# Kernel optimization log

Hardware: AMD Instinct MI355X
Metric: run time of the kernel (lower is better)

The kernel has to match this reference:

```python
import jax, jax.numpy as jnp
import numpy as np

N, E, B, D, F_IN, E_IN, H = 8192, 32768, 256, 64, 11, 5, 128


def setup_inputs() -> dict:
    key = jax.random.key(0)
    ks = jax.random.split(key, 32)
    rn = lambda k, shape, s: jax.random.normal(k, shape, jnp.float32) * s
    inp = {
        'x': jax.random.normal(ks[0], (N, F_IN), jnp.float32),
        'edge_attr': jax.random.uniform(ks[1], (E, E_IN), jnp.float32),
        'lin0_w': rn(ks[2], (D, F_IN), 0.3), 'lin0_b': jnp.zeros((D,), jnp.float32),
        'nn1_w': rn(ks[3], (H, E_IN), 0.4), 'nn1_b': jnp.zeros((H,), jnp.float32),
        'nn2_w': rn(ks[4], (D * D, H), 0.05), 'nn2_b': jnp.zeros((D * D,), jnp.float32),
        'root_w': rn(ks[5], (D, D), 0.125), 'conv_b': jnp.zeros((D,), jnp.float32),
        'gru_w_ih': rn(ks[6], (3 * D, D), 0.125), 'gru_w_hh': rn(ks[7], (3 * D, D), 0.125),
        'gru_b_ih': jnp.zeros((3 * D,), jnp.float32), 'gru_b_hh': jnp.zeros((3 * D,), jnp.float32),
        's2s_w_ih': rn(ks[8], (4 * D, 2 * D), 0.1), 's2s_w_hh': rn(ks[9], (4 * D, D), 0.125),
        's2s_b_ih': jnp.zeros((4 * D,), jnp.float32), 's2s_b_hh': jnp.zeros((4 * D,), jnp.float32),
        'lin1_w': rn(ks[10], (D, 2 * D), 0.1), 'lin1_b': jnp.zeros((D,), jnp.float32),
        'lin2_w': rn(ks[11], (1, D), 0.125), 'lin2_b': jnp.zeros((1,), jnp.float32),
        'edge_index': jax.random.randint(ks[12], (2, E), 0, N),
        'batch': jnp.sort(jax.random.randint(ks[13], (N,), 0, B)),
    }
    return inp


def _forward(x, edge_attr, lin0_w, lin0_b, nn1_w, nn1_b, nn2_w, nn2_b, root_w, conv_b,
             gru_w_ih, gru_w_hh, gru_b_ih, gru_b_hh, s2s_w_ih, s2s_w_hh, s2s_b_ih, s2s_b_hh,
             lin1_w, lin1_b, lin2_w, lin2_b, edge_index, batch):
    src, dst = edge_index[0], edge_index[1]
    # edge-conditioned weights: MLP(edge_attr) -> [E, D, D]; edge_attr is fixed,
    # so compute once (identical math to calling conv.nn each iteration)
    W_e = (jax.nn.relu(edge_attr @ nn1_w.T + nn1_b) @ nn2_w.T + nn2_b).reshape(E, D, D)
    deg = jax.ops.segment_sum(jnp.ones((E,), jnp.float32), dst, num_segments=N)
    inv_deg = jnp.where(deg > 0, 1.0 / jnp.maximum(deg, 1.0), 0.0)[:, None]  # [N,1]

    out = jax.nn.relu(x @ lin0_w.T + lin0_b)  # [N, D]
    h = out
    for _ in range(3):
        # NNConv: gather src features, per-edge matmul, scatter-mean to dst, + root + bias
        msg = jnp.einsum('ed,edf->ef', out[src], W_e)  # [E, D]
        agg = jax.ops.segment_sum(msg, dst, num_segments=N) * inv_deg
        m = jax.nn.relu(agg + out @ root_w.T + conv_b)
        # single-step GRU (torch GRU equations)
        gx = m @ gru_w_ih.T + gru_b_ih
        gh = h @ gru_w_hh.T + gru_b_hh
        xr, xz, xn = jnp.split(gx, 3, axis=-1)
        hr, hz, hn = jnp.split(gh, 3, axis=-1)
        r = jax.nn.sigmoid(xr + hr)
        z = jax.nn.sigmoid(xz + hz)
        n = jnp.tanh(xn + r * hn)
        h = (1.0 - z) * n + z * h
        out = h

    # Set2Set pooling, 3 processing steps
    qh = jnp.zeros((B, D), jnp.float32)
    qc = jnp.zeros((B, D), jnp.float32)
    q_star = jnp.zeros((B, 2 * D), jnp.float32)
    for _ in range(3):
        gates = q_star @ s2s_w_ih.T + s2s_b_ih + qh @ s2s_w_hh.T + s2s_b_hh
        gi, gf, gg, go = jnp.split(gates, 4, axis=-1)
        qc = jax.nn.sigmoid(gf) * qc + jax.nn.sigmoid(gi) * jnp.tanh(gg)
        qh = jax.nn.sigmoid(go) * jnp.tanh(qc)
        q = qh  # [B, D]
        e = jnp.sum(out * q[batch], axis=-1)  # [N]
        emax = jax.ops.segment_max(e, batch, num_segments=B)
        emax = jnp.where(jnp.isfinite(emax), emax, 0.0)
        a = jnp.exp(e - emax[batch])
        a_sum = jax.ops.segment_sum(a, batch, num_segments=B)
        a = a / jnp.maximum(a_sum, 1e-12)[batch]
        r_vec = jax.ops.segment_sum(a[:, None] * out, batch, num_segments=B)  # [B, D]
        q_star = jnp.concatenate([q, r_vec], axis=-1)

    y = jax.nn.relu(q_star @ lin1_w.T + lin1_b) @ lin2_w.T + lin2_b
    return y.reshape(-1)  # [B]


def reference(x, edge_attr, lin0_w, lin0_b, nn1_w, nn1_b, nn2_w, nn2_b, root_w, conv_b,
              gru_w_ih, gru_w_hh, gru_b_ih, gru_b_hh, s2s_w_ih, s2s_w_hh, s2s_b_ih, s2s_b_hh,
              lin1_w, lin1_b, lin2_w, lin2_b, edge_index, batch):
    return _forward(x, edge_attr, lin0_w, lin0_b, nn1_w, nn1_b, nn2_w, nn2_b, root_w, conv_b,
                    gru_w_ih, gru_w_hh, gru_b_ih, gru_b_hh, s2s_w_ih, s2s_w_hh, s2s_b_ih, s2s_b_hh,
                    lin1_w, lin1_b, lin2_w, lin2_b, edge_index, batch)
```

## Files before the change

kernel.cpp:

```cpp
#include <hip/hip_runtime.h>
#include <hip/hip_bf16.h>
#include <stdint.h>

#define NN 8192
#define EE 32768
#define BB 256
#define DD 64
#define FIN 11
#define EIN 5
#define HH 128

typedef __attribute__((ext_vector_type(4))) float f32x4;
typedef __attribute__((ext_vector_type(8))) short bf16x8;

__device__ __forceinline__ float sigmoidf_(float x) { return 1.0f / (1.0f + expf(-x)); }

__device__ __forceinline__ void gload16(const void* g, void* l) {
    __builtin_amdgcn_global_load_lds(
        (const __attribute__((address_space(1))) unsigned int*)g,
        (__attribute__((address_space(3))) unsigned int*)l, 16, 0, 0);
}

__global__ __launch_bounds__(256) void k_setup(const float* __restrict__ x,
                                               const float* __restrict__ edge_attr,
                                               const float* __restrict__ lin0_w,
                                               const float* __restrict__ lin0_b,
                                               const float* __restrict__ nn1_w,
                                               const float* __restrict__ nn1_b,
                                               const float* __restrict__ nn2_w,
                                               const float* __restrict__ nn2b,
                                               const float* __restrict__ root_w,
                                               const float* __restrict__ whh,
                                               const float* __restrict__ bhh,
                                               const float* __restrict__ s2s_wih,
                                               const float* __restrict__ s2s_whh,
                                               const int* __restrict__ ei,
                                               const int* __restrict__ batch,
                                               __hip_bfloat16* __restrict__ h1,
                                               float* __restrict__ outN,
                                               __hip_bfloat16* __restrict__ nn2T,
                                               float* __restrict__ wihT,
                                               float* __restrict__ whhT,
                                               float* __restrict__ Bcat,
                                               float* __restrict__ bcat,
                                               int* __restrict__ deg,
                                               int* __restrict__ cnt) {
    const int bid = blockIdx.x, t = threadIdx.x;
    if (bid < 16384) {
        int idx = bid * 256 + t;
        int e = idx >> 7, k = idx & 127;
        float a = nn1_b[k];
#pragma unroll
        for (int j = 0; j < EIN; j++) a += edge_attr[e * EIN + j] * nn1_w[k * EIN + j];
        h1[idx] = __float2bfloat16(fmaxf(a, 0.0f));
    } else if (bid < 18432) {
        int idx = (bid - 16384) * 256 + t;
        int n = idx >> 6, d = idx & 63;
        float a = lin0_b[d];
#pragma unroll
        for (int k = 0; k < FIN; k++) a += x[n * FIN + k] * lin0_w[d * FIN + k];
        outN[idx] = fmaxf(a, 0.0f);
    } else if (bid < 18688) {
        int u = (bid - 18432) * 256 + t;
        int d = u >> 10, rem = u & 1023, slot = rem >> 6, f = rem & 63;
        const float* src = nn2_w + ((size_t)(d * 64 + f) * 128 + slot * 8);
        float4 v0 = *(const float4*)(src);
        float4 v1 = *(const float4*)(src + 4);
        union { bf16x8 v; ushort us[8]; } ov;
        __hip_bfloat16 b;
        b = __float2bfloat16(v0.x); ov.us[0] = *(ushort*)&b;
        b = __float2bfloat16(v0.y); ov.us[1] = *(ushort*)&b;
        b = __float2bfloat16(v0.z); ov.us[2] = *(ushort*)&b;
        b = __float2bfloat16(v0.w); ov.us[3] = *(ushort*)&b;
        b = __float2bfloat16(v1.x); ov.us[4] = *(ushort*)&b;
        b = __float2bfloat16(v1.y); ov.us[5] = *(ushort*)&b;
        b = __float2bfloat16(v1.z); ov.us[6] = *(ushort*)&b;
        b = __float2bfloat16(v1.w); ov.us[7] = *(ushort*)&b;
        *(bf16x8*)((ushort*)nn2T + (size_t)u * 8) = ov.v;
    } else if (bid < 18880) {
        int i = (bid - 18688) * 256 + t;
        if (i < 256 * 128) {
            int j = i >> 7, k = i & 127;
            wihT[k * 256 + j] = s2s_wih[i];
        } else {
            int i2 = i - 256 * 128;
            if (i2 < 256 * 64) {
                int j = i2 >> 6, k = i2 & 63;
                whhT[k * 256 + j] = s2s_whh[i2];
            }
        }
    } else if (bid < 18960) {
        int i = (bid - 18880) * 256 + t;
        int r = i >> 6, c = i & 63;
        float v;
        if (r < 64) v = root_w[i];
        else if (r < 256) v = whh[(size_t)(r - 64) * 64 + c];
        else v = nn2b[c * 64 + (r - 256)];
        Bcat[i] = v;
        if (c == 0) bcat[r] = (r >= 64 && r < 256) ? bhh[r - 64] : 0.0f;
    } else {
        int i = (bid - 18960) * 256 + t;
        if (i < EE) atomicAdd(&deg[ei[EE + i]], 1);
        if (i < NN) atomicAdd(&cnt[batch[i]], 1);
    }
}

__global__ __launch_bounds__(256) void k_invscan(const int* __restrict__ deg,
                                                 float* __restrict__ invd,
                                                 const int* __restrict__ cnt,
                                                 int* __restrict__ offs) {
    const int bid = blockIdx.x, t = threadIdx.x;
    if (bid < 32) {
        int n = bid * 256 + t;
        int d = deg[n];
        invd[n] = d > 0 ? 1.0f / (float)d : 0.0f;
    } else {
        __shared__ int s[256];
        s[t] = cnt[t];
        __syncthreads();
        for (int off = 1; off < 256; off <<= 1) {
            int v = (t >= off) ? s[t - off] : 0;
            __syncthreads();
            s[t] += v;
            __syncthreads();
        }
        offs[t + 1] = s[t];
        if (t == 0) offs[0] = 0;
    }
}

__global__ __launch_bounds__(512, 6) void k_wemsg(const __hip_bfloat16* __restrict__ h1,
                                                  const __hip_bfloat16* __restrict__ nn2T,
                                                  const float* __restrict__ outN,
                                                  const float* __restrict__ rgh,
                                                  const int* __restrict__ ei,
                                                  const float* __restrict__ invd,
                                                  float* __restrict__ agg) {
    __shared__ ushort sB[2][64 * 128];
    __shared__ float soT[32][64];
    __shared__ int sDst[64];
    __shared__ int sSrc[64];
    __shared__ float sIv[64];

    const int t = threadIdx.x;
    const int w = t >> 6, l = t & 63;
    const int q = l >> 4, l15 = l & 15;
    const int eh = w >> 2, fs = (w & 3) * 16;
    const int e0 = (blockIdx.x >> 1) * 64;
    const int dh = blockIdx.x & 1;
    const int cbase = dh * 32;

    {
        int r = t >> 3, seg = t & 7;
        int s_ = ei[e0 + r];
        float4 v = *(const float4*)(outN + (size_t)s_ * 64 + dh * 32 + seg * 4);
        soT[seg * 4 + 0][r] = v.x;
        soT[seg * 4 + 1][r] = v.y;
        soT[seg * 4 + 2][r] = v.z;
        soT[seg * 4 + 3][r] = v.w;
        if (seg == 0) {
            int d_ = ei[EE + e0 + r];
            sDst[r] = d_;
            sIv[r] = invd[d_];
            sSrc[r] = s_;
        }
    }
    bf16x8 af[2][4];
#pragma unroll
    for (int mi = 0; mi < 2; mi++)
#pragma unroll
        for (int kk = 0; kk < 4; kk++)
            af[mi][kk] = *(const bf16x8*)(h1 + (size_t)(e0 + eh * 32 + mi * 16 + l15) * 128 + (kk * 4 + q) * 8);

    const __hip_bfloat16* p0 = nn2T + (size_t)cbase * 8192 + (size_t)t * 8;
    const __hip_bfloat16* p1 = nn2T + (size_t)cbase * 8192 + (size_t)(512 + t) * 8;
    ushort* d0a = &sB[0][(w * 64) * 8];
    ushort* d0b = &sB[0][(512 + w * 64) * 8];
    ushort* d1a = &sB[1][(w * 64) * 8];
    ushort* d1b = &sB[1][(512 + w * 64) * 8];

    gload16(p0, d0a);
    gload16(p1, d0b);
    __syncthreads();

    float msg[2][4];
#pragma unroll
    for (int mi = 0; mi < 2; mi++)
#pragma unroll
        for (int j = 0; j < 4; j++) msg[mi][j] = 0.0f;

    const int rb = fs + l15;
    const int lo0 = ((0 * 4 + q) * 64 + rb) * 8;
    const int lo1 = ((1 * 4 + q) * 64 + rb) * 8;
    const int lo2 = ((2 * 4 + q) * 64 + rb) * 8;
    const int lo3 = ((3 * 4 + q) * 64 + rb) * 8;

    for (int dl = 0; dl < 32; ++dl) {
        const int cur = dl & 1;
        if (dl < 31) {
            size_t off = (size_t)(dl + 1) * 8192;
            gload16(p0 + off, cur ? d0a : d1a);
            gload16(p1 + off, cur ? d0b : d1b);
        }
        const ushort* sbc = &sB[cur][0];
        f32x4 a0 = (f32x4)0.0f, a1 = (f32x4)0.0f;
        {
            bf16x8 b0_ = *(const bf16x8*)&sbc[lo0];
            a0 = __builtin_amdgcn_mfma_f32_16x16x32_bf16(af[0][0], b0_, a0, 0, 0, 0);
            a1 = __builtin_amdgcn_mfma_f32_16x16x32_bf16(af[1][0], b0_, a1, 0, 0, 0);
            bf16x8 b1_ = *(const bf16x8*)&sbc[lo1];
            a0 = __builtin_amdgcn_mfma_f32_16x16x32_bf16(af[0][1], b1_, a0, 0, 0, 0);
            a1 = __builtin_amdgcn_mfma_f32_16x16x32_bf16(af[1][1], b1_, a1, 0, 0, 0);
            bf16x8 b2_ = *(const bf16x8*)&sbc[lo2];
            a0 = __builtin_amdgcn_mfma_f32_16x16x32_bf16(af[0][2], b2_, a0, 0, 0, 0);
            a1 = __builtin_amdgcn_mfma_f32_16x16x32_bf16(af[1][2], b2_, a1, 0, 0, 0);
            bf16x8 b3_ = *(const bf16x8*)&sbc[lo3];
            a0 = __builtin_amdgcn_mfma_f32_16x16x32_bf16(af[0][3], b3_, a0, 0, 0, 0);
            a1 = __builtin_amdgcn_mfma_f32_16x16x32_bf16(af[1][3], b3_, a1, 0, 0, 0);
        }
        {
            f32x4 s0 = *(const f32x4*)&soT[dl][eh * 32 + q * 4];
            f32x4 s1 = *(const f32x4*)&soT[dl][eh * 32 + 16 + q * 4];
#pragma unroll
            for (int j = 0; j < 4; j++) {
                msg[0][j] += a0[j] * s0[j];
                msg[1][j] += a1[j] * s1[j];
            }
        }
        __syncthreads();
    }

    const int fcol = fs + l15;
#pragma unroll
    for (int mi = 0; mi < 2; mi++) {
#pragma unroll
        for (int j = 0; j < 4; j++) {
            int er = eh * 32 + mi * 16 + q * 4 + j;
            float v = msg[mi][j];
            if (dh == 0) v += rgh[(size_t)sSrc[er] * 320 + 256 + fcol];
            atomicAdd(&agg[(size_t)sDst[er] * 64 + fcol], v * sIv[er]);
        }
    }
}

__global__ __launch_bounds__(256) void k_rgh(const float* __restrict__ A,
                                             const float* __restrict__ Bm,
                                             const float* __restrict__ bias,
                                             float* __restrict__ C,
                                             float* __restrict__ aggz) {
    const int tid = threadIdx.x;
    const int bx = blockIdx.x, by = blockIdx.y;
    {
        int bid = by * 5 + bx;
        if (bid < 512) {
            float4 z; z.x = z.y = z.z = z.w = 0.0f;
            *(float4*)(aggz + (size_t)bid * 1024 + tid * 4) = z;
        }
    }
    __shared__ float sA[64 * 68];
    __shared__ float sB[64 * 68];
    const float* Ab = A + (size_t)by * 64 * 64;
    const float* Bb = Bm + (size_t)bx * 64 * 64;
    for (int fi = tid; fi < 64 * 16; fi += 256) {
        int r = fi >> 4, c = (fi & 15) * 4;
        *(float4*)&sA[r * 68 + c] = *(const float4*)(Ab + (size_t)r * 64 + c);
        *(float4*)&sB[r * 68 + c] = *(const float4*)(Bb + (size_t)r * 64 + c);
    }
    __syncthreads();
    const int tx = tid & 15, ty = tid >> 4;
    float acc[4][4];
#pragma unroll
    for (int i = 0; i < 4; i++)
#pragma unroll
        for (int j = 0; j < 4; j++) acc[i][j] = 0.0f;
    for (int k = 0; k < 64; k += 4) {
        float4 av[4], bv[4];
#pragma unroll
        for (int i = 0; i < 4; i++) av[i] = *(const float4*)&sA[(ty + 16 * i) * 68 + k];
#pragma unroll
        for (int j = 0; j < 4; j++) bv[j] = *(const float4*)&sB[(tx + 16 * j) * 68 + k];
#pragma unroll
        for (int i = 0; i < 4; i++)
#pragma unroll
            for (int j = 0; j < 4; j++) {
                acc[i][j] += av[i].x * bv[j].x;
                acc[i][j] += av[i].y * bv[j].y;
                acc[i][j] += av[i].z * bv[j].z;
                acc[i][j] += av[i].w * bv[j].w;
            }
    }
#pragma unroll
    for (int i = 0; i < 4; i++) {
        size_t row = (size_t)by * 64 + ty + 16 * i;
#pragma unroll
        for (int j = 0; j < 4; j++) {
            int col = bx * 64 + tx + 16 * j;
            C[row * 320 + col] = acc[i][j] + bias[col];
        }
    }
}

__global__ __launch_bounds__(256) void k_gxgru(const float* __restrict__ agg,
                                               const float* __restrict__ rgh,
                                               const float* __restrict__ cb,
                                               const float* __restrict__ wih,
                                               const float* __restrict__ bih,
                                               float* __restrict__ outN) {
    __shared__ float sA[64 * 68];
    __shared__ float sB[192 * 68];
    const int t = threadIdx.x;
    const int by = blockIdx.x;
    for (int fi = t; fi < 64 * 16; fi += 256) {
        int r = fi >> 4, c = (fi & 15) * 4;
        float4 av = *(const float4*)(agg + (size_t)(by * 64 + r) * 64 + c);
        float4 rv = *(const float4*)(rgh + (size_t)(by * 64 + r) * 320 + c);
        float4 cv = *(const float4*)(cb + c);
        float4 m;
        m.x = fmaxf(av.x + rv.x + cv.x, 0.0f);
        m.y = fmaxf(av.y + rv.y + cv.y, 0.0f);
        m.z = fmaxf(av.z + rv.z + cv.z, 0.0f);
        m.w = fmaxf(av.w + rv.w + cv.w, 0.0f);
        *(float4*)&sA[r * 68 + c] = m;
    }
    for (int fi = t; fi < 192 * 16; fi += 256) {
        int r = fi >> 4, c = (fi & 15) * 4;
        *(float4*)&sB[r * 68 + c] = *(const float4*)(wih + (size_t)r * 64 + c);
    }
    __syncthreads();
    const int tx = t & 15, ty = t >> 4;
    float acc[3][4][4];
#pragma unroll
    for (int cx = 0; cx < 3; cx++)
#pragma unroll
        for (int i = 0; i < 4; i++)
#pragma unroll
            for (int j = 0; j < 4; j++) acc[cx][i][j] = 0.0f;
    for (int k = 0; k < 64; k += 4) {
        float4 av[4];
#pragma unroll
        for (int i = 0; i < 4; i++) av[i] = *(const float4*)&sA[(ty + 16 * i) * 68 + k];
#pragma unroll
        for (int cx = 0; cx < 3; cx++) {
            float4 bv[4];
#pragma unroll
            for (int j = 0; j < 4; j++) bv[j] = *(const float4*)&sB[(cx * 64 + tx + 16 * j) * 68 + k];
#pragma unroll
            for (int i = 0; i < 4; i++)
#pragma unroll
                for (int j = 0; j < 4; j++) {
                    acc[cx][i][j] += av[i].x * bv[j].x;
                    acc[cx][i][j] += av[i].y * bv[j].y;
                    acc[cx][i][j] += av[i].z * bv[j].z;
                    acc[cx][i][j] += av[i].w * bv[j].w;
                }
        }
    }
#pragma unroll
    for (int i = 0; i < 4; i++) {
        int n = by * 64 + ty + 16 * i;
        const float* ghr = rgh + (size_t)n * 320 + 64;
#pragma unroll
        for (int j = 0; j < 4; j++) {
            int d = tx + 16 * j;
            float r = sigmoidf_(acc[0][i][j] + bih[d] + ghr[d]);
            float z = sigmoidf_(acc[1][i][j] + bih[64 + d] + ghr[64 + d]);
            float nn_ = tanhf(acc[2][i][j] + bih[128 + d] + r * ghr[128 + d]);
            float hp = outN[(size_t)n * 64 + d];
            outN[(size_t)n * 64 + d] = (1.0f - z) * nn_ + z * hp;
        }
    }
}

__global__ __launch_bounds__(256) void k_s2sall(const float* __restrict__ outN,
                                                const int* __restrict__ offs,
                                                const float* __restrict__ wihT,
                                                const float* __restrict__ whhT,
                                                const float* __restrict__ bih,
                                                const float* __restrict__ bhh,
                                                const float* __restrict__ lin1_w,
                                                const float* __restrict__ lin1_b,
                                                const float* __restrict__ lin2_w,
                                                const float* __restrict__ lin2_b,
                                                float* __restrict__ earr,
                                                float* __restrict__ y) {
    const int b = blockIdx.x, t = threadIdx.x;
    const int w = t >> 6, l = t & 63;
    __shared__ float qs[128], qhL[64], qcL[64], gates[256];
    __shared__ float red[8];
    __shared__ float rpart[4][64];
    __shared__ float hbuf[64];
    const int s0 = offs[b], s1 = offs[b + 1];
    if (t < 128) qs[t] = 0.0f;
    if (t < 64) { qhL[t] = 0.0f; qcL[t] = 0.0f; }
    __syncthreads();

    for (int st = 0; st < 3; st++) {
        float g = bih[t] + bhh[t];
        for (int k = 0; k < 128; k++) g += qs[k] * wihT[k * 256 + t];
        for (int k = 0; k < 64; k++) g += qhL[k] * whhT[k * 256 + t];
        gates[t] = g;
        __syncthreads();
        if (t < 64) {
            float gi = gates[t], gf = gates[64 + t], gg = gates[128 + t], go = gates[192 + t];
            float c = sigmoidf_(gf) * qcL[t] + sigmoidf_(gi) * tanhf(gg);
            qcL[t] = c;
            qhL[t] = sigmoidf_(go) * tanhf(c);
        }
        __syncthreads();
        float mx = -INFINITY;
        for (int i = s0 + w; i < s1; i += 4) {
            float p = outN[(size_t)i * 64 + l] * qhL[l];
#pragma unroll
            for (int o = 32; o > 0; o >>= 1) p += __shfl_xor(p, o, 64);
            if (l == 0) earr[i] = p;
            mx = fmaxf(mx, p);
        }
        if (l == 0) red[w] = mx;
        __syncthreads();
        mx = fmaxf(fmaxf(red[0], red[1]), fmaxf(red[2], red[3]));
        if (!isfinite(mx)) mx = 0.0f;
        float sm = 0.0f, racc = 0.0f;
        for (int i = s0 + w; i < s1; i += 4) {
            float a = expf(earr[i] - mx);
            sm += a;
            racc += a * outN[(size_t)i * 64 + l];
        }
        rpart[w][l] = racc;
        if (l == 0) red[4 + w] = sm;
        __syncthreads();
        float smT = fmaxf(red[4] + red[5] + red[6] + red[7], 1e-12f);
        if (t < 64) {
            float r = (rpart[0][t] + rpart[1][t] + rpart[2][t] + rpart[3][t]) / smT;
            qs[t] = qhL[t];
            qs[64 + t] = r;
        }
        __syncthreads();
    }
    if (t < 64) {
        float h = lin1_b[t];
        for (int k = 0; k < 128; k++) h += qs[k] * lin1_w[t * 128 + k];
        hbuf[t] = fmaxf(h, 0.0f) * lin2_w[t];
    }
    __syncthreads();
    if (w == 0) {
        float p = hbuf[l];
#pragma unroll
        for (int o = 32; o > 0; o >>= 1) p += __shfl_xor(p, o, 64);
        if (l == 0) y[b] = p + lin2_b[0];
    }
}

extern "C" void kernel_launch(void* const* d_in, const int* in_sizes, int n_in,
                              void* d_out, int out_size, void* d_ws, size_t ws_size,
                              hipStream_t stream) {
    const float* x = (const float*)d_in[0];
    const float* edge_attr = (const float*)d_in[1];
    const float* lin0_w = (const float*)d_in[2];
    const float* lin0_b = (const float*)d_in[3];
    const float* nn1_w = (const float*)d_in[4];
    const float* nn1_b = (const float*)d_in[5];
    const float* nn2_w = (const float*)d_in[6];
    const float* nn2_b = (const float*)d_in[7];
    const float* root_w = (const float*)d_in[8];
    const float* conv_b = (const float*)d_in[9];
    const float* gru_w_ih = (const float*)d_in[10];
    const float* gru_w_hh = (const float*)d_in[11];
    const float* gru_b_ih = (const float*)d_in[12];
    const float* gru_b_hh = (const float*)d_in[13];
    const float* s2s_w_ih = (const float*)d_in[14];
    const float* s2s_w_hh = (const float*)d_in[15];
    const float* s2s_b_ih = (const float*)d_in[16];
    const float* s2s_b_hh = (const float*)d_in[17];
    const float* lin1_w = (const float*)d_in[18];
    const float* lin1_b = (const float*)d_in[19];
    const float* lin2_w = (const float*)d_in[20];
    const float* lin2_b = (const float*)d_in[21];
    const int* ei = (const int*)d_in[22];
    const int* batch = (const int*)d_in[23];
    float* outp = (float*)d_out;

    char* w = (char*)d_ws;
    auto carve = [&](size_t bytes) { char* p = w; w += (bytes + 255) & ~(size_t)255; return p; };
    __hip_bfloat16* nn2T = (__hip_bfloat16*)carve((size_t)4096 * 128 * 2);
    float* outN = (float*)carve((size_t)NN * 64 * 4);
    __hip_bfloat16* h1 = (__hip_bfloat16*)carve((size_t)EE * 128 * 2);
    int* deg = (int*)carve(NN * 4);
    float* invd = (float*)carve(NN * 4);
    float* agg = (float*)carve((size_t)NN * 64 * 4);
    float* rgh = (float*)carve((size_t)NN * 320 * 4);
    float* Bcat = (float*)carve((size_t)320 * 64 * 4);
    float* bcat = (float*)carve(320 * 4);
    float* wihT = (float*)carve((size_t)128 * 256 * 4);
    float* whhT = (float*)carve((size_t)64 * 256 * 4);
    float* earr = (float*)carve(NN * 4);
    int* cnt = (int*)carve(256 * 4);
    int* offs = (int*)carve(257 * 4);

    hipMemsetAsync(deg, 0, NN * 4, stream);
    hipMemsetAsync(cnt, 0, 256 * 4, stream);

    k_setup<<<19088, 256, 0, stream>>>(x, edge_attr, lin0_w, lin0_b, nn1_w, nn1_b,
                                       nn2_w, nn2_b, root_w, gru_w_hh, gru_b_hh,
                                       s2s_w_ih, s2s_w_hh, ei, batch,
                                       h1, outN, nn2T, wihT, whhT, Bcat, bcat, deg, cnt);
    k_invscan<<<33, 256, 0, stream>>>(deg, invd, cnt, offs);

    for (int it = 0; it < 3; it++) {
        k_rgh<<<dim3(5, NN / 64), 256, 0, stream>>>(outN, Bcat, bcat, rgh, agg);
        k_wemsg<<<EE / 32, 512, 0, stream>>>(h1, nn2T, outN, rgh, ei, invd, agg);
        k_gxgru<<<NN / 64, 256, 0, stream>>>(agg, rgh, conv_b, gru_w_ih, gru_b_ih, outN);
    }

    k_s2sall<<<BB, 256, 0, stream>>>(outN, offs, wihT, whhT, s2s_b_ih, s2s_b_hh,
                                     lin1_w, lin1_b, lin2_w, lin2_b, earr, outp);
}
```

Before: 321.8 us.

## Halve wemsg block to 256 threads with 4 edge tiles per wave; vectorize setup

The edge-message kernel now runs 4 waves per block instead of 8, and each wave computes all 64 edges (four 16-row MFMA tiles) for its 16 output columns. Each B fragment read from LDS is therefore reused across four MFMAs instead of two, which cuts LDS traffic per FLOP. The cost is more accumulator and A-fragment registers per wave and fewer waves per block to hide latency. Separately, the setup kernel computes 4 outputs per thread with vector stores for h1 and outN, which reduces its block count.

Result: slower. 336.7 us (+4.6%).

```diff
diff --git a/kernel.cpp b/kernel.cpp
--- a/kernel.cpp
+++ b/kernel.cpp
@@ -46,22 +46,41 @@
                                                int* __restrict__ deg,
                                                int* __restrict__ cnt) {
     const int bid = blockIdx.x, t = threadIdx.x;
-    if (bid < 16384) {
-        int idx = bid * 256 + t;
-        int e = idx >> 7, k = idx & 127;
-        float a = nn1_b[k];
-#pragma unroll
-        for (int j = 0; j < EIN; j++) a += edge_attr[e * EIN + j] * nn1_w[k * EIN + j];
-        h1[idx] = __float2bfloat16(fmaxf(a, 0.0f));
-    } else if (bid < 18432) {
-        int idx = (bid - 16384) * 256 + t;
-        int n = idx >> 6, d = idx & 63;
-        float a = lin0_b[d];
-#pragma unroll
-        for (int k = 0; k < FIN; k++) a += x[n * FIN + k] * lin0_w[d * FIN + k];
-        outN[idx] = fmaxf(a, 0.0f);
-    } else if (bid < 18688) {
-        int u = (bid - 18432) * 256 + t;
+    if (bid < 4096) {
+        int u = bid * 256 + t;
+        int e = u >> 5, k0 = (u & 31) * 4;
+        float ea0 = edge_attr[e * EIN + 0], ea1 = edge_attr[e * EIN + 1],
+              ea2 = edge_attr[e * EIN + 2], ea3 = edge_attr[e * EIN + 3],
+              ea4 = edge_attr[e * EIN + 4];
+        ushort4 o;
+#pragma unroll
+        for (int kk = 0; kk < 4; kk++) {
+            int k = k0 + kk;
+            const float* wr = nn1_w + k * EIN;
+            float a = nn1_b[k] + ea0 * wr[0] + ea1 * wr[1] + ea2 * wr[2] + ea3 * wr[3] + ea4 * wr[4];
+            __hip_bfloat16 b = __float2bfloat16(fmaxf(a, 0.0f));
+            ((ushort*)&o)[kk] = *(ushort*)&b;
+        }
+        *(ushort4*)((ushort*)h1 + (size_t)e * 128 + k0) = o;
+    } else if (bid < 4608) {
+        int u = (bid - 4096) * 256 + t;
+        int n = u >> 4, d0 = (u & 15) * 4;
+        float xv[FIN];
+#pragma unroll
+        for (int k = 0; k < FIN; k++) xv[k] = x[n * FIN + k];
+        float4 o;
+#pragma unroll
+        for (int dd = 0; dd < 4; dd++) {
+            int d = d0 + dd;
+            const float* wr = lin0_w + d * FIN;
+            float a = lin0_b[d];
+#pragma unroll
+            for (int k = 0; k < FIN; k++) a += xv[k] * wr[k];
+            ((float*)&o)[dd] = fmaxf(a, 0.0f);
+        }
+        *(float4*)(outN + (size_t)n * 64 + d0) = o;
+    } else if (bid < 4864) {
+        int u = (bid - 4608) * 256 + t;
         int d = u >> 10, rem = u & 1023, slot = rem >> 6, f = rem & 63;
         const float* src = nn2_w + ((size_t)(d * 64 + f) * 128 + slot * 8);
         float4 v0 = *(const float4*)(src);
@@ -77,8 +96,8 @@
         b = __float2bfloat16(v1.z); ov.us[6] = *(ushort*)&b;
         b = __float2bfloat16(v1.w); ov.us[7] = *(ushort*)&b;
         *(bf16x8*)((ushort*)nn2T + (size_t)u * 8) = ov.v;
-    } else if (bid < 18880) {
-        int i = (bid - 18688) * 256 + t;
+    } else if (bid < 5056) {
+        int i = (bid - 4864) * 256 + t;
         if (i < 256 * 128) {
             int j = i >> 7, k = i & 127;
             wihT[k * 256 + j] = s2s_wih[i];
@@ -89,8 +108,8 @@
                 whhT[k * 256 + j] = s2s_whh[i2];
             }
         }
-    } else if (bid < 18960) {
-        int i = (bid - 18880) * 256 + t;
+    } else if (bid < 5136) {
+        int i = (bid - 5056) * 256 + t;
         int r = i >> 6, c = i & 63;
         float v;
         if (r < 64) v = root_w[i];
@@ -99,7 +118,7 @@
         Bcat[i] = v;
         if (c == 0) bcat[r] = (r >= 64 && r < 256) ? bhh[r - 64] : 0.0f;
     } else {
-        int i = (bid - 18960) * 256 + t;
+        int i = (bid - 5136) * 256 + t;
         if (i < EE) atomicAdd(&deg[ei[EE + i]], 1);
         if (i < NN) atomicAdd(&cnt[batch[i]], 1);
     }
@@ -129,7 +148,7 @@
     }
 }
 
-__global__ __launch_bounds__(512, 6) void k_wemsg(const __hip_bfloat16* __restrict__ h1,
+__global__ __launch_bounds__(256, 3) void k_wemsg(const __hip_bfloat16* __restrict__ h1,
                                                   const __hip_bfloat16* __restrict__ nn2T,
                                                   const float* __restrict__ outN,
                                                   const float* __restrict__ rgh,
@@ -145,19 +164,25 @@
     const int t = threadIdx.x;
     const int w = t >> 6, l = t & 63;
     const int q = l >> 4, l15 = l & 15;
-    const int eh = w >> 2, fs = (w & 3) * 16;
     const int e0 = (blockIdx.x >> 1) * 64;
     const int dh = blockIdx.x & 1;
     const int cbase = dh * 32;
 
     {
-        int r = t >> 3, seg = t & 7;
+        int r = t >> 2, seg = t & 3;
         int s_ = ei[e0 + r];
-        float4 v = *(const float4*)(outN + (size_t)s_ * 64 + dh * 32 + seg * 4);
-        soT[seg * 4 + 0][r] = v.x;
-        soT[seg * 4 + 1][r] = v.y;
-        soT[seg * 4 + 2][r] = v.z;
-        soT[seg * 4 + 3][r] = v.w;
+        const float* orow = outN + (size_t)s_ * 64 + dh * 32 + seg * 8;
+        float4 v0 = *(const float4*)(orow);
+        float4 v1 = *(const float4*)(orow + 4);
+        int c0 = seg * 8;
+        soT[c0 + 0][r] = v0.x;
+        soT[c0 + 1][r] = v0.y;
+        soT[c0 + 2][r] = v0.z;
+        soT[c0 + 3][r] = v0.w;
+        soT[c0 + 4][r] = v1.x;
+        soT[c0 + 5][r] = v1.y;
+        soT[c0 + 6][r] = v1.z;
+        soT[c0 + 7][r] = v1.w;
         if (seg == 0) {
             int d_ = ei[EE + e0 + r];
             sDst[r] = d_;
@@ -165,31 +190,26 @@
             sSrc[r] = s_;
         }
     }
-    bf16x8 af[2][4];
-#pragma unroll
-    for (int mi = 0; mi < 2; mi++)
+    bf16x8 af[4][4];
+#pragma unroll
+    for (int mi = 0; mi < 4; mi++)
 #pragma unroll
         for (int kk = 0; kk < 4; kk++)
-            af[mi][kk] = *(const bf16x8*)(h1 + (size_t)(e0 + eh * 32 + mi * 16 + l15) * 128 + (kk * 4 + q) * 8);
-
-    const __hip_bfloat16* p0 = nn2T + (size_t)cbase * 8192 + (size_t)t * 8;
-    const __hip_bfloat16* p1 = nn2T + (size_t)cbase * 8192 + (size_t)(512 + t) * 8;
-    ushort* d0a = &sB[0][(w * 64) * 8];
-    ushort* d0b = &sB[0][(512 + w * 64) * 8];
-    ushort* d1a = &sB[1][(w * 64) * 8];
-    ushort* d1b = &sB[1][(512 + w * 64) * 8];
-
-    gload16(p0, d0a);
-    gload16(p1, d0b);
+            af[mi][kk] = *(const bf16x8*)(h1 + (size_t)(e0 + mi * 16 + l15) * 128 + (kk * 4 + q) * 8);
+
+    const __hip_bfloat16* pst = nn2T + (size_t)cbase * 8192 + (size_t)t * 8;
+#pragma unroll
+    for (int i = 0; i < 4; i++)
+        gload16(pst + i * 2048, &sB[0][(i * 256 + w * 64) * 8]);
     __syncthreads();
 
-    float msg[2][4];
-#pragma unroll
-    for (int mi = 0; mi < 2; mi++)
+    float msg[4][4];
+#pragma unroll
+    for (int mi = 0; mi < 4; mi++)
 #pragma unroll
         for (int j = 0; j < 4; j++) msg[mi][j] = 0.0f;
 
-    const int rb = fs + l15;
+    const int rb = w * 16 + l15;
     const int lo0 = ((0 * 4 + q) * 64 + rb) * 8;
     const int lo1 = ((1 * 4 + q) * 64 + rb) * 8;
     const int lo2 = ((2 * 4 + q) * 64 + rb) * 8;
@@ -199,43 +219,57 @@
         const int cur = dl & 1;
         if (dl < 31) {
             size_t off = (size_t)(dl + 1) * 8192;
-            gload16(p0 + off, cur ? d0a : d1a);
-            gload16(p1 + off, cur ? d0b : d1b);
+            ushort* db = cur ? &sB[0][0] : &sB[1][0];
+#pragma unroll
+            for (int i = 0; i < 4; i++)
+                gload16(pst + off + i * 2048, db + (i * 256 + w * 64) * 8);
         }
         const ushort* sbc = &sB[cur][0];
-        f32x4 a0 = (f32x4)0.0f, a1 = (f32x4)0.0f;
+        f32x4 a0 = (f32x4)0.0f, a1 = (f32x4)0.0f, a2 = (f32x4)0.0f, a3 = (f32x4)0.0f;
         {
             bf16x8 b0_ = *(const bf16x8*)&sbc[lo0];
             a0 = __builtin_amdgcn_mfma_f32_16x16x32_bf16(af[0][0], b0_, a0, 0, 0, 0);
             a1 = __builtin_amdgcn_mfma_f32_16x16x32_bf16(af[1][0], b0_, a1, 0, 0, 0);
+            a2 = __builtin_amdgcn_mfma_f32_16x16x32_bf16(af[2][0], b0_, a2, 0, 0, 0);
+            a3 = __builtin_amdgcn_mfma_f32_16x16x32_bf16(af[3][0], b0_, a3, 0, 0, 0);
             bf16x8 b1_ = *(const bf16x8*)&sbc[lo1];
             a0 = __builtin_amdgcn_mfma_f32_16x16x32_bf16(af[0][1], b1_, a0, 0, 0, 0);
             a1 = __builtin_amdgcn_mfma_f32_16x16x32_bf16(af[1][1], b1_, a1, 0, 0, 0);
+            a2 = __builtin_amdgcn_mfma_f32_16x16x32_bf16(af[2][1], b1_, a2, 0, 0, 0);
+            a3 = __builtin_amdgcn_mfma_f32_16x16x32_bf16(af[3][1], b1_, a3, 0, 0, 0);
             bf16x8 b2_ = *(const bf16x8*)&sbc[lo2];
             a0 = __builtin_amdgcn_mfma_f32_16x16x32_bf16(af[0][2], b2_, a0, 0, 0, 0);
             a1 = __builtin_amdgcn_mfma_f32_16x16x32_bf16(af[1][2], b2_, a1, 0, 0, 0);
+            a2 = __builtin_amdgcn_mfma_f32_16x16x32_bf16(af[2][2], b2_, a2, 0, 0, 0);
+            a3 = __builtin_amdgcn_mfma_f32_16x16x32_bf16(af[3][2], b2_, a3, 0, 0, 0);
             bf16x8 b3_ = *(const bf16x8*)&sbc[lo3];
             a0 = __builtin_amdgcn_mfma_f32_16x16x32_bf16(af[0][3], b3_, a0, 0, 0, 0);
             a1 = __builtin_amdgcn_mfma_f32_16x16x32_bf16(af[1][3], b3_, a1, 0, 0, 0);
+            a2 = __builtin_amdgcn_mfma_f32_16x16x32_bf16(af[2][3], b3_, a2, 0, 0, 0);
+            a3 = __builtin_amdgcn_mfma_f32_16x16x32_bf16(af[3][3], b3_, a3, 0, 0, 0);
         }
         {
-            f32x4 s0 = *(const f32x4*)&soT[dl][eh * 32 + q * 4];
-            f32x4 s1 = *(const f32x4*)&soT[dl][eh * 32 + 16 + q * 4];
+            f32x4 s0 = *(const f32x4*)&soT[dl][0 * 16 + q * 4];
+            f32x4 s1 = *(const f32x4*)&soT[dl][1 * 16 + q * 4];
+            f32x4 s2 = *(const f32x4*)&soT[dl][2 * 16 + q * 4];
+            f32x4 s3 = *(const f32x4*)&soT[dl][3 * 16 + q * 4];
 #pragma unroll
             for (int j = 0; j < 4; j++) {
                 msg[0][j] += a0[j] * s0[j];
                 msg[1][j] += a1[j] * s1[j];
+                msg[2][j] += a2[j] * s2[j];
+                msg[3][j] += a3[j] * s3[j];
             }
         }
         __syncthreads();
     }
 
-    const int fcol = fs + l15;
-#pragma unroll
-    for (int mi = 0; mi < 2; mi++) {
+    const int fcol = w * 16 + l15;
+#pragma unroll
+    for (int mi = 0; mi < 4; mi++) {
 #pragma unroll
         for (int j = 0; j < 4; j++) {
-            int er = eh * 32 + mi * 16 + q * 4 + j;
+            int er = mi * 16 + q * 4 + j;
             float v = msg[mi][j];
             if (dh == 0) v += rgh[(size_t)sSrc[er] * 320 + 256 + fcol];
             atomicAdd(&agg[(size_t)sDst[er] * 64 + fcol], v * sIv[er]);
@@ -499,15 +533,15 @@
     hipMemsetAsync(deg, 0, NN * 4, stream);
     hipMemsetAsync(cnt, 0, 256 * 4, stream);
 
-    k_setup<<<19088, 256, 0, stream>>>(x, edge_attr, lin0_w, lin0_b, nn1_w, nn1_b,
-                                       nn2_w, nn2_b, root_w, gru_w_hh, gru_b_hh,
-                                       s2s_w_ih, s2s_w_hh, ei, batch,
-                                       h1, outN, nn2T, wihT, whhT, Bcat, bcat, deg, cnt);
+    k_setup<<<5264, 256, 0, stream>>>(x, edge_attr, lin0_w, lin0_b, nn1_w, nn1_b,
+                                      nn2_w, nn2_b, root_w, gru_w_hh, gru_b_hh,
+                                      s2s_w_ih, s2s_w_hh, ei, batch,
+                                      h1, outN, nn2T, wihT, whhT, Bcat, bcat, deg, cnt);
     k_invscan<<<33, 256, 0, stream>>>(deg, invd, cnt, offs);
 
     for (int it = 0; it < 3; it++) {
         k_rgh<<<dim3(5, NN / 64), 256, 0, stream>>>(outN, Bcat, bcat, rgh, agg);
-        k_wemsg<<<EE / 32, 512, 0, stream>>>(h1, nn2T, outN, rgh, ei, invd, agg);
+        k_wemsg<<<EE / 32, 256, 0, stream>>>(h1, nn2T, outN, rgh, ei, invd, agg);
         k_gxgru<<<NN / 64, 256, 0, stream>>>(agg, rgh, conv_b, gru_w_ih, gru_b_ih, outN);
     }
 
```
